# Optimization experiments

Measured on AMD Instinct MI355X. Metric: run time of the kernel, lower is better.

## Reference

```python
import jax, jax.numpy as jnp
import numpy as np

OUTDIM = 10
STRIDES = (2, 2, 1)
PADS = (2, 2, 1)  # int((k-1)/2) for k=5,5,3
LEAK = 0.2


def _conv(x, w, b, s, p):
    y = jax.lax.conv_general_dilated(x, w, (s, s), [(p, p), (p, p)],
                                     dimension_numbers=('NCHW', 'OIHW', 'NCHW'))
    return y + b[None, :, None, None]


def _grid(outdim):
    off = (jnp.arange(outdim, dtype=jnp.float32) - (outdim - 1) / 2.0) / outdim
    gx = jnp.broadcast_to(off[None, :], (outdim, outdim))  # varies along j (x)
    gy = jnp.broadcast_to(off[:, None], (outdim, outdim))  # varies along i (y)
    return jnp.stack([gx, gy], axis=-1)  # [od, od, 2]


def _bilinear(img, x, y):
    # img: [C,H,W]; x,y: [N] float. Faithful to original (x clamped by H, y by W).
    H, W = img.shape[-2], img.shape[-1]
    x0 = jnp.floor(x).astype(jnp.int32); x1 = x0 + 1
    y0 = jnp.floor(y).astype(jnp.int32); y1 = y0 + 1
    x0 = jnp.clip(x0, 0, H - 1); x1 = jnp.clip(x1, 0, H - 1)
    y0 = jnp.clip(y0, 0, W - 1); y1 = jnp.clip(y1, 0, W - 1)
    Ia = img[:, y0, x0]; Ib = img[:, y1, x0]; Ic = img[:, y0, x1]; Id = img[:, y1, x1]
    x0f = x0.astype(x.dtype); x1f = x1.astype(x.dtype)
    y0f = y0.astype(y.dtype); y1f = y1.astype(y.dtype)
    step = jnp.clip((x1f - x0f) * (y1f - y0f), 0.001, 2.0)
    inv = 1.0 / step
    wa = (x1f - x) * (y1f - y) * inv
    wb = (x1f - x) * (y - y0f) * inv
    wc = (x - x0f) * (y1f - y) * inv
    wd = (x - x0f) * (y - y0f) * inv
    return Ia * wa + Ib * wb + Ic * wc + Id * wd  # [C, N]


def _roi_one(feat, roi, gg):
    # feat: [C,H,W]; roi: [R,7]
    W1, W2 = roi[:, 2:3], roi[:, 3:4]
    H1, H2 = roi[:, 4:5], roi[:, 5:6]
    psi = roi[:, 6:7]
    WH = jnp.concatenate([W1 + W2, H1 + H2], axis=-1)          # [R,2]
    offset = jnp.concatenate([(W1 - W2) / 2, (H1 - H2) / 2], axis=-1)
    s, c = jnp.sin(psi), jnp.cos(psi)                          # [R,1]
    rotM = jnp.stack([jnp.concatenate([c, -s], -1),
                      jnp.concatenate([s, c], -1)], axis=-2)   # [R,2,2]
    ggi = gg[None] * WH[:, None, None, :] - offset[:, None, None, :]  # [R,od,od,2]
    ggi = jnp.einsum('rijk,rkl->rijl', ggi, rotM) + roi[:, None, None, 0:2]
    xs = ggi[..., 0].reshape(-1)
    ys = ggi[..., 1].reshape(-1)
    samp = _bilinear(feat, xs, ys)                             # [C, R*od*od]
    R, C = roi.shape[0], feat.shape[0]
    # faithful to original .view(R, C, od, od) applied to the [C, N] buffer
    return samp.reshape(R, C, OUTDIM, OUTDIM)


def setup_inputs() -> dict:
    key = jax.random.key(0)
    ks = jax.random.split(key, 12)
    B, R = 32, 32
    x = jax.random.normal(ks[0], (B, 3, 224, 224), dtype=jnp.float32)
    u = jax.random.uniform(ks[1], (B, R, 7), dtype=jnp.float32)
    lo = jnp.array([5., 5., 1., 1., 1., 1., -np.pi], dtype=jnp.float32)
    hi = jnp.array([51., 51., 8., 8., 8., 8., np.pi], dtype=jnp.float32)
    ROI = lo + u * (hi - lo)  # coords in 56x56 feature-map frame
    w1 = jax.random.normal(ks[2], (32, 3, 5, 5), dtype=jnp.float32) * 0.05
    b1 = jnp.zeros((32,), dtype=jnp.float32)
    w2 = jax.random.normal(ks[3], (64, 32, 5, 5), dtype=jnp.float32) * 0.05
    b2 = jnp.zeros((64,), dtype=jnp.float32)
    w3 = jax.random.normal(ks[4], (128, 64, 3, 3), dtype=jnp.float32) * 0.05
    b3 = jnp.zeros((128,), dtype=jnp.float32)
    fc_w = jax.random.normal(ks[5], (256, OUTDIM * OUTDIM * 128), dtype=jnp.float32) * 0.01
    fc_b = jnp.zeros((256,), dtype=jnp.float32)
    return {'x': x, 'ROI': ROI, 'w1': w1, 'b1': b1, 'w2': w2, 'b2': b2,
            'w3': w3, 'b3': b3, 'fc_w': fc_w, 'fc_b': fc_b}


def reference(x, ROI, w1, b1, w2, b2, w3, b3, fc_w, fc_b):
    for (w, b, s, p) in ((w1, b1, STRIDES[0], PADS[0]),
                         (w2, b2, STRIDES[1], PADS[1]),
                         (w3, b3, STRIDES[2], PADS[2])):
        x = jax.nn.leaky_relu(_conv(x, w, b, s, p), LEAK)
    gg = _grid(OUTDIM)
    roi_feat = jax.vmap(lambda f, r: _roi_one(f, r, gg))(x, ROI)  # [B,R,C,od,od]
    B, R = roi_feat.shape[0], roi_feat.shape[1]
    flat = roi_feat.reshape(B, R, -1)
    return flat @ fc_w.T + fc_b  # [B, R, 256]
```

## Files before the change

### kernel.cpp

```cpp
#include <hip/hip_runtime.h>
#include <hip/hip_bf16.h>

#define LEAK 0.2f

__device__ __forceinline__ float lrelu(float a) { return a > 0.0f ? a : LEAK * a; }

typedef __attribute__((ext_vector_type(8))) short short8;
typedef __attribute__((ext_vector_type(4))) float f32x4;

__device__ __forceinline__ unsigned short bf16_hi_bits(float x) {
    unsigned u = __builtin_bit_cast(unsigned, x);
    unsigned r = u + 0x7fffu + ((u >> 16) & 1u);
    return (unsigned short)(r >> 16);
}
__device__ __forceinline__ float bf16_to_f32(unsigned short h) {
    unsigned u = ((unsigned)h) << 16;
    return __builtin_bit_cast(float, u);
}
__device__ __forceinline__ unsigned pack_bf16pair(float x) {
    unsigned short h = bf16_hi_bits(x);
    float lo = x - bf16_to_f32(h);
    return (unsigned)h | ((unsigned)bf16_hi_bits(lo) << 16);
}

__device__ __forceinline__ unsigned pack_lo16(unsigned o, unsigned e) {
    return __builtin_amdgcn_perm(o, e, 0x05040100u);
}
__device__ __forceinline__ unsigned pack_hi16(unsigned o, unsigned e) {
    return __builtin_amdgcn_perm(o, e, 0x07060302u);
}

template<int CO, int KIN, int KP>
__global__ __launch_bounds__(256) void wtr_pack_k(const float* __restrict__ w,
                                                  unsigned* __restrict__ wTp) {
    int i = blockIdx.x * 256 + threadIdx.x;
    if (i >= KP * CO) return;
    int k = i / CO, co = i % CO;
    float x = (k < KIN) ? w[(size_t)co * KIN + k] : 0.0f;
    wTp[i] = pack_bf16pair(x);
}

__global__ __launch_bounds__(256) void split_pack_k(const float* __restrict__ src,
                                                    unsigned* __restrict__ dst, int n) {
    for (int i = blockIdx.x * 256 + threadIdx.x; i < n; i += gridDim.x * 256) {
        dst[i] = pack_bf16pair(src[i]);
    }
}

__global__ __launch_bounds__(256, 4) void conv1_mfma_k(
    const unsigned* __restrict__ src,
    const unsigned* __restrict__ wp,
    const float* __restrict__ bias,
    unsigned* __restrict__ outp)
{
    __shared__ unsigned ldsu[6400];
    __shared__ int offtab[96];
    short* const lds = (short*)ldsu;

    const int tid  = threadIdx.x;
    const int lane = tid & 63;
    const int wv   = tid >> 6;
    const int bx   = blockIdx.x;
    const int bz   = blockIdx.y;

    if (tid < 96) {
        int k = min(tid, 74);
        int ci = k / 25, r = k - ci * 25;
        int kh = r / 5, kw = r - kh * 5;
        offtab[tid] = (ci * 228 + kh) * 228 + kw;
    }
    __syncthreads();

    const int brow = tid & 127, half = tid >> 7;
    const int bn   = bx * 128 + brow;
    const int boh  = bn / 112, bow = bn % 112;
    const unsigned* __restrict__ bsrc =
        src + ((size_t)(bz * 3) * 228 + boh * 2) * 228 + bow * 2;
    const int arow = tid & 31, ks = (tid >> 5) & 3;

    unsigned Bu[16], Au[8];
    auto gather = [&](int it) {
        const int k0 = it * 32;
#pragma unroll
        for (int c = 0; c < 2; ++c) {
            int kb = k0 + (half * 2 + c) * 8;
            int4 o0 = *(const int4*)&offtab[kb];
            int4 o1 = *(const int4*)&offtab[kb + 4];
            Bu[c * 8 + 0] = bsrc[o0.x]; Bu[c * 8 + 1] = bsrc[o0.y];
            Bu[c * 8 + 2] = bsrc[o0.z]; Bu[c * 8 + 3] = bsrc[o0.w];
            Bu[c * 8 + 4] = bsrc[o1.x]; Bu[c * 8 + 5] = bsrc[o1.y];
            Bu[c * 8 + 6] = bsrc[o1.z]; Bu[c * 8 + 7] = bsrc[o1.w];
        }
        if (tid < 128) {
            const unsigned* __restrict__ wk = wp + (size_t)(k0 + ks * 8) * 32 + arow;
#pragma unroll
            for (int j = 0; j < 8; ++j) Au[j] = wk[j * 32];
        }
    };

    f32x4 acc[2][2] = {};
    const int r15 = lane & 15, kg = lane >> 4;

    gather(0);
    for (int it = 0; it < 3; ++it) {
        {
            uint4 vh, vl;
#pragma unroll
            for (int c = 0; c < 2; ++c) {
                vh.x = pack_lo16(Bu[c*8+1], Bu[c*8+0]); vl.x = pack_hi16(Bu[c*8+1], Bu[c*8+0]);
                vh.y = pack_lo16(Bu[c*8+3], Bu[c*8+2]); vl.y = pack_hi16(Bu[c*8+3], Bu[c*8+2]);
                vh.z = pack_lo16(Bu[c*8+5], Bu[c*8+4]); vl.z = pack_hi16(Bu[c*8+5], Bu[c*8+4]);
                vh.w = pack_lo16(Bu[c*8+7], Bu[c*8+6]); vl.w = pack_hi16(Bu[c*8+7], Bu[c*8+6]);
                *(uint4*)&ldsu[1280 + brow * 20 + (half * 2 + c) * 4] = vh;
                *(uint4*)&ldsu[3840 + brow * 20 + (half * 2 + c) * 4] = vl;
            }
            if (tid < 128) {
                vh.x = pack_lo16(Au[1], Au[0]); vl.x = pack_hi16(Au[1], Au[0]);
                vh.y = pack_lo16(Au[3], Au[2]); vl.y = pack_hi16(Au[3], Au[2]);
                vh.z = pack_lo16(Au[5], Au[4]); vl.z = pack_hi16(Au[5], Au[4]);
                vh.w = pack_lo16(Au[7], Au[6]); vl.w = pack_hi16(Au[7], Au[6]);
                *(uint4*)&ldsu[arow * 20 + ks * 4]       = vh;
                *(uint4*)&ldsu[640 + arow * 20 + ks * 4] = vl;
            }
        }
        __syncthreads();
        if (it + 1 < 3) gather(it + 1);

        const short* AsH = lds;
        const short* AsL = lds + 1280;
        const short* BsH = lds + 2560;
        const short* BsL = lds + 7680;
        short8 aH[2], aL[2], bH[2], bL[2];
#pragma unroll
        for (int tq = 0; tq < 2; ++tq) {
            const int ra = (tq * 16 + r15) * 40 + kg * 8;
            aH[tq] = *(const short8*)&AsH[ra];
            aL[tq] = *(const short8*)&AsL[ra];
            const int rb = (wv * 32 + tq * 16 + r15) * 40 + kg * 8;
            bH[tq] = *(const short8*)&BsH[rb];
            bL[tq] = *(const short8*)&BsL[rb];
        }
#pragma unroll
        for (int ct = 0; ct < 2; ++ct)
#pragma unroll
            for (int pt = 0; pt < 2; ++pt) {
                acc[ct][pt] = __builtin_amdgcn_mfma_f32_16x16x32_bf16(aH[ct], bH[pt], acc[ct][pt], 0, 0, 0);
                acc[ct][pt] = __builtin_amdgcn_mfma_f32_16x16x32_bf16(aH[ct], bL[pt], acc[ct][pt], 0, 0, 0);
                acc[ct][pt] = __builtin_amdgcn_mfma_f32_16x16x32_bf16(aL[ct], bH[pt], acc[ct][pt], 0, 0, 0);
            }
        __syncthreads();
    }

#pragma unroll
    for (int ct = 0; ct < 2; ++ct)
#pragma unroll
        for (int pt = 0; pt < 2; ++pt)
#pragma unroll
            for (int rg = 0; rg < 4; ++rg) {
                int co = ct * 16 + kg * 4 + rg;
                int px = bx * 128 + wv * 32 + pt * 16 + r15;
                int poh = px / 112, pw_ = px % 112;
                float v = acc[ct][pt][rg] + bias[co];
                outp[((size_t)(bz * 32 + co) * 116 + poh + 2) * 120 + pw_ + 4] =
                    pack_bf16pair(lrelu(v));
            }
}

template<int CI, int ST, int KH, int KW, int KP,
         int PIH, int PIW, int LP,
         int CO, int OW, int OSH, int OSW, int OR0, int OC0, bool POUT>
__global__ __launch_bounds__(256, 4) void conv_mfma_k(
    const unsigned* __restrict__ src,
    const unsigned* __restrict__ wp,
    const float* __restrict__ bias,
    void* __restrict__ outv)
{
    constexpr int KT = KP / 32;
    __shared__ unsigned ldsu[5120];
    __shared__ int offtab[KP];
    short* const lds = (short*)ldsu;

    const int tid  = threadIdx.x;
    const int lane = tid & 63;
    const int wv   = tid >> 6;
    const int bx   = blockIdx.x;
    const int by   = blockIdx.y;
    const int bz   = blockIdx.z;

    for (int k = tid; k < KP; k += 256) {
        int ci = k / (KH * KW), r = k - ci * (KH * KW);
        int kh = r / KW, kw = r - kh * KW;
        offtab[k] = (ci * PIH + kh) * PIW + kw;
    }
    __syncthreads();

    const int row = lane;
    const int n   = bx * 64 + row;
    const int oh  = n / OW, ow = n % OW;
    const unsigned* __restrict__ bsrc =
        src + ((size_t)(bz * CI) * PIH + oh * ST) * PIW + ow * ST + LP;
    const unsigned* __restrict__ wsrc = wp + (size_t)(wv * 8) * CO + by * 64 + row;

    unsigned Au[8], Bu[8];
    auto gather = [&](int it) {
        const int k0 = it * 32 + wv * 8;
        int4 o0 = *(const int4*)&offtab[k0];
        int4 o1 = *(const int4*)&offtab[k0 + 4];
        const unsigned* __restrict__ wk = wsrc + (size_t)it * 32 * CO;
#pragma unroll
        for (int j = 0; j < 8; ++j) Au[j] = wk[j * CO];
        Bu[0] = bsrc[o0.x]; Bu[1] = bsrc[o0.y]; Bu[2] = bsrc[o0.z]; Bu[3] = bsrc[o0.w];
        Bu[4] = bsrc[o1.x]; Bu[5] = bsrc[o1.y]; Bu[6] = bsrc[o1.z]; Bu[7] = bsrc[o1.w];
    };

    f32x4 acc[2][2] = {};

    const int cw = wv & 1, pw = wv >> 1;
    const int r15 = lane & 15, kg = lane >> 4;

    gather(0);
    for (int it = 0; it < KT; ++it) {
        {
            const int widx = row * 20 + wv * 4;
            uint4 vh, vl;
            vh.x = pack_lo16(Au[1], Au[0]); vl.x = pack_hi16(Au[1], Au[0]);
            vh.y = pack_lo16(Au[3], Au[2]); vl.y = pack_hi16(Au[3], Au[2]);
            vh.z = pack_lo16(Au[5], Au[4]); vl.z = pack_hi16(Au[5], Au[4]);
            vh.w = pack_lo16(Au[7], Au[6]); vl.w = pack_hi16(Au[7], Au[6]);
            *(uint4*)&ldsu[0 * 1280 + widx] = vh;
            *(uint4*)&ldsu[1 * 1280 + widx] = vl;
            vh.x = pack_lo16(Bu[1], Bu[0]); vl.x = pack_hi16(Bu[1], Bu[0]);
            vh.y = pack_lo16(Bu[3], Bu[2]); vl.y = pack_hi16(Bu[3], Bu[2]);
            vh.z = pack_lo16(Bu[5], Bu[4]); vl.z = pack_hi16(Bu[5], Bu[4]);
            vh.w = pack_lo16(Bu[7], Bu[6]); vl.w = pack_hi16(Bu[7], Bu[6]);
            *(uint4*)&ldsu[2 * 1280 + widx] = vh;
            *(uint4*)&ldsu[3 * 1280 + widx] = vl;
        }
        __syncthreads();
        if (it + 1 < KT) gather(it + 1);

        const short* AsH = lds + 0 * 2560;
        const short* AsL = lds + 1 * 2560;
        const short* BsH = lds + 2 * 2560;
        const short* BsL = lds + 3 * 2560;
        short8 aH[2], aL[2], bH[2], bL[2];
#pragma unroll
        for (int tq = 0; tq < 2; ++tq) {
            const int ra = (cw * 32 + tq * 16 + r15) * 40 + kg * 8;
            aH[tq] = *(const short8*)&AsH[ra];
            aL[tq] = *(const short8*)&AsL[ra];
            const int rb = (pw * 32 + tq * 16 + r15) * 40 + kg * 8;
            bH[tq] = *(const short8*)&BsH[rb];
            bL[tq] = *(const short8*)&BsL[rb];
        }
#pragma unroll
        for (int ct = 0; ct < 2; ++ct)
#pragma unroll
            for (int pt = 0; pt < 2; ++pt) {
                acc[ct][pt] = __builtin_amdgcn_mfma_f32_16x16x32_bf16(aH[ct], bH[pt], acc[ct][pt], 0, 0, 0);
                acc[ct][pt] = __builtin_amdgcn_mfma_f32_16x16x32_bf16(aH[ct], bL[pt], acc[ct][pt], 0, 0, 0);
                acc[ct][pt] = __builtin_amdgcn_mfma_f32_16x16x32_bf16(aL[ct], bH[pt], acc[ct][pt], 0, 0, 0);
            }
        __syncthreads();
    }

#pragma unroll
    for (int ct = 0; ct < 2; ++ct)
#pragma unroll
        for (int pt = 0; pt < 2; ++pt)
#pragma unroll
            for (int rg = 0; rg < 4; ++rg) {
                int co = by * 64 + cw * 32 + ct * 16 + kg * 4 + rg;
                int px = bx * 64 + pw * 32 + pt * 16 + r15;
                int poh = px / OW, pow_ = px % OW;
                float v = lrelu(acc[ct][pt][rg] + bias[co]);
                size_t off = ((size_t)(bz * CO + co) * OSH + (poh + OR0)) * OSW + (pow_ + OC0);
                if (POUT) ((unsigned*)outv)[off] = pack_bf16pair(v);
                else      ((float*)outv)[off]    = v;
            }
}

__global__ __launch_bounds__(256, 4) void fc_mfma_k(
    const unsigned* __restrict__ Sp,
    const unsigned* __restrict__ Wp,
    float* __restrict__ part)
{
    __shared__ unsigned ldsu[7680];
    short* const lds = (short*)ldsu;

    const int tid  = threadIdx.x;
    const int lane = tid & 63;
    const int wv   = tid >> 6;
    const int bn = blockIdx.x, bm = blockIdx.y, ks = blockIdx.z;

    const int ra = tid & 127, ca = tid >> 7;
    const int rb = tid & 63,  cb = tid >> 6;
    const unsigned* __restrict__ aptr = Sp + (size_t)(bm * 128 + ra) * 12800 + ks * 800;
    const unsigned* __restrict__ bptr = Wp + (size_t)(bn * 64 + rb) * 12800 + ks * 800;

    unsigned Au[16], Bu[8];
    auto gather = [&](int it) {
        const int k0 = it * 32;
#pragma unroll
        for (int j = 0; j < 8; ++j) {
            Au[j]     = aptr[k0 + ca * 8 + j];
            Au[8 + j] = aptr[k0 + (ca + 2) * 8 + j];
            Bu[j]     = bptr[k0 + cb * 8 + j];
        }
    };

    f32x4 acc[2][4] = {};
    const int r15 = lane & 15, kg = lane >> 4;

    gather(0);
    for (int it = 0; it < 25; ++it) {
        {
            uint4 vh, vl;
            vh.x = pack_lo16(Au[1], Au[0]); vl.x = pack_hi16(Au[1], Au[0]);
            vh.y = pack_lo16(Au[3], Au[2]); vl.y = pack_hi16(Au[3], Au[2]);
            vh.z = pack_lo16(Au[5], Au[4]); vl.z = pack_hi16(Au[5], Au[4]);
            vh.w = pack_lo16(Au[7], Au[6]); vl.w = pack_hi16(Au[7], Au[6]);
            *(uint4*)&ldsu[ra * 20 + ca * 4]        = vh;
            *(uint4*)&ldsu[2560 + ra * 20 + ca * 4] = vl;
            vh.x = pack_lo16(Au[9],  Au[8]);  vl.x = pack_hi16(Au[9],  Au[8]);
            vh.y = pack_lo16(Au[11], Au[10]); vl.y = pack_hi16(Au[11], Au[10]);
            vh.z = pack_lo16(Au[13], Au[12]); vl.z = pack_hi16(Au[13], Au[12]);
            vh.w = pack_lo16(Au[15], Au[14]); vl.w = pack_hi16(Au[15], Au[14]);
            *(uint4*)&ldsu[ra * 20 + (ca + 2) * 4]        = vh;
            *(uint4*)&ldsu[2560 + ra * 20 + (ca + 2) * 4] = vl;
            vh.x = pack_lo16(Bu[1], Bu[0]); vl.x = pack_hi16(Bu[1], Bu[0]);
            vh.y = pack_lo16(Bu[3], Bu[2]); vl.y = pack_hi16(Bu[3], Bu[2]);
            vh.z = pack_lo16(Bu[5], Bu[4]); vl.z = pack_hi16(Bu[5], Bu[4]);
            vh.w = pack_lo16(Bu[7], Bu[6]); vl.w = pack_hi16(Bu[7], Bu[6]);
            *(uint4*)&ldsu[5120 + rb * 20 + cb * 4] = vh;
            *(uint4*)&ldsu[6400 + rb * 20 + cb * 4] = vl;
        }
        __syncthreads();
        if (it + 1 < 25) gather(it + 1);

        const short* AsH = lds;
        const short* AsL = AsH + 5120;
        const short* BsH = AsH + 10240;
        const short* BsL = AsH + 12800;
        short8 aH[2], aL[2], bH[4], bL[4];
#pragma unroll
        for (int mq = 0; mq < 2; ++mq) {
            const int rr = (wv * 32 + mq * 16 + r15) * 40 + kg * 8;
            aH[mq] = *(const short8*)&AsH[rr];
            aL[mq] = *(const short8*)&AsL[rr];
        }
#pragma unroll
        for (int nq = 0; nq < 4; ++nq) {
            const int rr = (nq * 16 + r15) * 40 + kg * 8;
            bH[nq] = *(const short8*)&BsH[rr];
            bL[nq] = *(const short8*)&BsL[rr];
        }
#pragma unroll
        for (int mq = 0; mq < 2; ++mq)
#pragma unroll
            for (int nq = 0; nq < 4; ++nq) {
                acc[mq][nq] = __builtin_amdgcn_mfma_f32_16x16x32_bf16(aH[mq], bH[nq], acc[mq][nq], 0, 0, 0);
                acc[mq][nq] = __builtin_amdgcn_mfma_f32_16x16x32_bf16(aH[mq], bL[nq], acc[mq][nq], 0, 0, 0);
                acc[mq][nq] = __builtin_amdgcn_mfma_f32_16x16x32_bf16(aL[mq], bH[nq], acc[mq][nq], 0, 0, 0);
            }
        __syncthreads();
    }

    float* __restrict__ po = part + (size_t)ks * 262144;
#pragma unroll
    for (int mq = 0; mq < 2; ++mq)
#pragma unroll
        for (int nq = 0; nq < 4; ++nq)
#pragma unroll
            for (int rg = 0; rg < 4; ++rg) {
                int m = bm * 128 + wv * 32 + mq * 16 + kg * 4 + rg;
                int ncol = bn * 64 + nq * 16 + r15;
                po[(size_t)m * 256 + ncol] = acc[mq][nq][rg];
            }
}

__global__ __launch_bounds__(256) void pad_x_k(const float* __restrict__ x,
                                               unsigned* __restrict__ xp) {
    int blk = blockIdx.x;
    int r4 = blk % 57, ic = blk / 57;
    int wid = threadIdx.x >> 6, lane = threadIdx.x & 63;
    int row = r4 * 4 + wid;
    const float* __restrict__ src = x + (size_t)ic * 224 * 224 + (size_t)(row - 2) * 224;
    unsigned* __restrict__ dst = xp + (size_t)ic * 228 * 228 + (size_t)row * 228;
    bool rok = (row >= 2) && (row < 226);
    for (int c = lane; c < 228; c += 64) {
        float v = 0.0f;
        if (rok && c >= 2 && c < 226) v = src[c - 2];
        dst[c] = pack_bf16pair(v);
    }
}

__global__ __launch_bounds__(256) void zb_c1p_k(float* __restrict__ p) {
    float* base = p + (size_t)blockIdx.x * (116 * 120);
    for (int t = threadIdx.x; t < 928; t += 256) {
        int idx;
        if (t < 480) {
            int r = t / 120, c = t - r * 120;
            int row = (r < 2) ? r : r + 112;
            idx = row * 120 + c;
        } else {
            int s = t - 480;
            int r = s >> 2, c = s & 3;
            int col = (c < 2) ? (c + 2) : (c + 114);
            idx = (r + 2) * 120 + col;
        }
        base[idx] = 0.0f;
    }
}

__global__ __launch_bounds__(64) void zb_c2p_k(float* __restrict__ p) {
    float* base = p + (size_t)blockIdx.x * (58 * 64);
    for (int t = threadIdx.x; t < 240; t += 64) {
        int idx;
        if (t < 128) {
            int r = t >> 6, c = t & 63;
            idx = (r ? 57 : 0) * 64 + c;
        } else {
            int s = t - 128;
            int r = (s >> 1) + 1;
            idx = r * 64 + ((s & 1) ? 60 : 3);
        }
        base[idx] = 0.0f;
    }
}

__global__ __launch_bounds__(256) void roi_k(const float* __restrict__ feat,
                                             const float* __restrict__ roi,
                                             unsigned* __restrict__ S) {
    int b = blockIdx.x >> 5;
    int r = blockIdx.x & 31;
    const float* rr = roi + (size_t)(b * 32 + r) * 7;

    __shared__ int   offA[100], offB[100], offC[100], offD[100];
    __shared__ float wA[100], wB[100], wC[100], wD[100];

    int tid = threadIdx.x;
    if (tid < 100) {
        int i = tid / 10, j = tid % 10;
        float cx = rr[0], cy = rr[1];
        float W1 = rr[2], W2 = rr[3], H1 = rr[4], H2 = rr[5], psi = rr[6];
        float offx = ((float)j - 4.5f) / 10.0f;
        float offy = ((float)i - 4.5f) / 10.0f;
        float gx = offx * (W1 + W2) - (W1 - W2) * 0.5f;
        float gy = offy * (H1 + H2) - (H1 - H2) * 0.5f;
        float sn = sinf(psi), cs = cosf(psi);
        float xs = gx * cs + gy * sn + cx;
        float ys = -gx * sn + gy * cs + cy;

        float x0f = floorf(xs), y0f = floorf(ys);
        int x0 = (int)x0f, x1 = x0 + 1;
        int y0 = (int)y0f, y1 = y0 + 1;
        x0 = min(max(x0, 0), 55); x1 = min(max(x1, 0), 55);
        y0 = min(max(y0, 0), 55); y1 = min(max(y1, 0), 55);
        float fx0 = (float)x0, fx1 = (float)x1;
        float fy0 = (float)y0, fy1 = (float)y1;
        float step = (fx1 - fx0) * (fy1 - fy0);
        step = fminf(fmaxf(step, 0.001f), 2.0f);
        float inv = 1.0f / step;
        wA[tid] = (fx1 - xs) * (fy1 - ys) * inv;
        wB[tid] = (fx1 - xs) * (ys - fy0) * inv;
        wC[tid] = (xs - fx0) * (fy1 - ys) * inv;
        wD[tid] = (xs - fx0) * (ys - fy0) * inv;
        offA[tid] = y0 * 56 + x0;
        offB[tid] = y1 * 56 + x0;
        offC[tid] = y0 * 56 + x1;
        offD[tid] = y1 * 56 + x1;
    }
    __syncthreads();

    const float* __restrict__ fb = feat + (size_t)b * 128 * 3136;
    unsigned* __restrict__ outb = S + ((size_t)b * 128 * 32 + r) * 100;
    int c = tid / 100;
    int p = tid - c * 100;
    for (int t = tid; t < 12800; t += 256) {
        const float* f = fb + c * 3136;
        float v = wA[p] * f[offA[p]] + wB[p] * f[offB[p]] +
                  wC[p] * f[offC[p]] + wD[p] * f[offD[p]];
        outb[(size_t)c * 3200 + p] = pack_bf16pair(v);
        p += 56; c += 2;
        if (p >= 100) { p -= 100; ++c; }
    }
}

__global__ __launch_bounds__(256) void fc2_reduce_k(const float* __restrict__ part,
                                                    const float* __restrict__ bias,
                                                    float* __restrict__ out) {
    int i = blockIdx.x * 256 + threadIdx.x;
    float s = bias[i & 255];
    for (int ks = 0; ks < 16; ++ks) s += part[(size_t)ks * 262144 + i];
    out[i] = s;
}

extern "C" void kernel_launch(void* const* d_in, const int* in_sizes, int n_in,
                              void* d_out, int out_size, void* d_ws, size_t ws_size,
                              hipStream_t stream) {
    const float* x   = (const float*)d_in[0];
    const float* ROI = (const float*)d_in[1];
    const float* w1  = (const float*)d_in[2];
    const float* b1  = (const float*)d_in[3];
    const float* w2  = (const float*)d_in[4];
    const float* b2  = (const float*)d_in[5];
    const float* w3  = (const float*)d_in[6];
    const float* b3  = (const float*)d_in[7];
    const float* fcw = (const float*)d_in[8];
    const float* fcb = (const float*)d_in[9];
    float* out = (float*)d_out;

    char* ws = (char*)d_ws;
    unsigned* c1p  = (unsigned*)(ws);
    unsigned* c2p  = (unsigned*)(ws + 57016320);
    unsigned* xpad = (unsigned*)(ws + 87425024);
    unsigned* wT1p = (unsigned*)(ws + 107386880);
    unsigned* wT2p = (unsigned*)(ws + 107399168);
    unsigned* wT3p = (unsigned*)(ws + 107603968);
    float* c3   = (float*)(ws);
    unsigned* S = (unsigned*)(ws + 57016320);
    unsigned* wfcp = (unsigned*)(ws);
    float* part = (float*)(ws + 16777216);

    wtr_pack_k<32, 75, 96><<<12, 256, 0, stream>>>(w1, wT1p);
    wtr_pack_k<64, 800, 800><<<200, 256, 0, stream>>>(w2, wT2p);
    wtr_pack_k<128, 576, 576><<<288, 256, 0, stream>>>(w3, wT3p);
    pad_x_k<<<32 * 3 * 57, 256, 0, stream>>>(x, xpad);
    zb_c1p_k<<<1024, 256, 0, stream>>>((float*)c1p);
    zb_c2p_k<<<2048, 64, 0, stream>>>((float*)c2p);

    conv1_mfma_k<<<dim3(98, 32), 256, 0, stream>>>(xpad, wT1p, b1, c1p);

    conv_mfma_k<32, 2, 5, 5, 800, 116, 120, 2, 64, 56, 58, 64, 1, 4, true>
        <<<dim3(49, 1, 32), 256, 0, stream>>>(c1p, wT2p, b2, c2p);

    conv_mfma_k<64, 1, 3, 3, 576, 58, 64, 3, 128, 56, 56, 56, 0, 0, false>
        <<<dim3(49, 2, 32), 256, 0, stream>>>(c2p, wT3p, b3, c3);

    roi_k<<<1024, 256, 0, stream>>>(c3, ROI, S);
    split_pack_k<<<4096, 256, 0, stream>>>(fcw, wfcp, 3276800);
    fc_mfma_k<<<dim3(4, 8, 16), 256, 0, stream>>>(S, wfcp, part);
    fc2_reduce_k<<<1024, 256, 0, stream>>>(part, fcb, out);
}
```

Before: 371.2 us.

## Widen conv MFMA pixel tile to 128 and flatten batch into pixel dimension

The generic conv2/conv3 implicit-GEMM kernel now covers 128 output pixels per block instead of 64, with each wave computing a 32x64 tile. The batch grid dimension is folded into a flat pixel index (PPI = 3136 pixels per image), so the image index is derived per pixel. This doubles reuse of each weight tile loaded into LDS and halves the block count. The cost is more LDS (7680 words), more accumulators and gather registers per thread, which may lower occupancy.

After: 382.1 us. 1.03x slower.

```diff
diff --git a/kernel.cpp b/kernel.cpp
--- a/kernel.cpp
+++ b/kernel.cpp
@@ -168,7 +168,7 @@
 
 template<int CI, int ST, int KH, int KW, int KP,
          int PIH, int PIW, int LP,
-         int CO, int OW, int OSH, int OSW, int OR0, int OC0, bool POUT>
+         int CO, int OW, int PPI, int OSH, int OSW, int OR0, int OC0, bool POUT>
 __global__ __launch_bounds__(256, 4) void conv_mfma_k(
     const unsigned* __restrict__ src,
     const unsigned* __restrict__ wp,
@@ -176,7 +176,7 @@
     void* __restrict__ outv)
 {
     constexpr int KT = KP / 32;
-    __shared__ unsigned ldsu[5120];
+    __shared__ unsigned ldsu[7680];
     __shared__ int offtab[KP];
     short* const lds = (short*)ldsu;
 
@@ -185,7 +185,6 @@
     const int wv   = tid >> 6;
     const int bx   = blockIdx.x;
     const int by   = blockIdx.y;
-    const int bz   = blockIdx.z;
 
     for (int k = tid; k < KP; k += 256) {
         int ci = k / (KH * KW), r = k - ci * (KH * KW);
@@ -194,26 +193,30 @@
     }
     __syncthreads();
 
-    const int row = lane;
-    const int n   = bx * 64 + row;
-    const int oh  = n / OW, ow = n % OW;
+    const int brow = tid & 127, khalf = tid >> 7;
+    const int bn   = bx * 128 + brow;
+    const int bimg = bn / PPI, brem = bn % PPI;
+    const int boh  = brem / OW, bow = brem % OW;
     const unsigned* __restrict__ bsrc =
-        src + ((size_t)(bz * CI) * PIH + oh * ST) * PIW + ow * ST + LP;
-    const unsigned* __restrict__ wsrc = wp + (size_t)(wv * 8) * CO + by * 64 + row;
-
-    unsigned Au[8], Bu[8];
+        src + ((size_t)(bimg * CI) * PIH + boh * ST) * PIW + bow * ST + LP;
+    const int arow = tid & 63, aks = tid >> 6;
+    const unsigned* __restrict__ wsrc = wp + (size_t)(aks * 8) * CO + by * 64 + arow;
+
+    unsigned Bu[16], Au[8];
     auto gather = [&](int it) {
-        const int k0 = it * 32 + wv * 8;
-        int4 o0 = *(const int4*)&offtab[k0];
-        int4 o1 = *(const int4*)&offtab[k0 + 4];
+        const int k0 = it * 32;
+#pragma unroll
+        for (int c = 0; c < 4; ++c) {
+            int4 o = *(const int4*)&offtab[k0 + khalf * 16 + c * 4];
+            Bu[c * 4 + 0] = bsrc[o.x]; Bu[c * 4 + 1] = bsrc[o.y];
+            Bu[c * 4 + 2] = bsrc[o.z]; Bu[c * 4 + 3] = bsrc[o.w];
+        }
         const unsigned* __restrict__ wk = wsrc + (size_t)it * 32 * CO;
 #pragma unroll
         for (int j = 0; j < 8; ++j) Au[j] = wk[j * CO];
-        Bu[0] = bsrc[o0.x]; Bu[1] = bsrc[o0.y]; Bu[2] = bsrc[o0.z]; Bu[3] = bsrc[o0.w];
-        Bu[4] = bsrc[o1.x]; Bu[5] = bsrc[o1.y]; Bu[6] = bsrc[o1.z]; Bu[7] = bsrc[o1.w];
     };
 
-    f32x4 acc[2][2] = {};
+    f32x4 acc[2][4] = {};
 
     const int cw = wv & 1, pw = wv >> 1;
     const int r15 = lane & 15, kg = lane >> 4;
@@ -221,42 +224,47 @@
     gather(0);
     for (int it = 0; it < KT; ++it) {
         {
-            const int widx = row * 20 + wv * 4;
             uint4 vh, vl;
             vh.x = pack_lo16(Au[1], Au[0]); vl.x = pack_hi16(Au[1], Au[0]);
             vh.y = pack_lo16(Au[3], Au[2]); vl.y = pack_hi16(Au[3], Au[2]);
             vh.z = pack_lo16(Au[5], Au[4]); vl.z = pack_hi16(Au[5], Au[4]);
             vh.w = pack_lo16(Au[7], Au[6]); vl.w = pack_hi16(Au[7], Au[6]);
-            *(uint4*)&ldsu[0 * 1280 + widx] = vh;
-            *(uint4*)&ldsu[1 * 1280 + widx] = vl;
-            vh.x = pack_lo16(Bu[1], Bu[0]); vl.x = pack_hi16(Bu[1], Bu[0]);
-            vh.y = pack_lo16(Bu[3], Bu[2]); vl.y = pack_hi16(Bu[3], Bu[2]);
-            vh.z = pack_lo16(Bu[5], Bu[4]); vl.z = pack_hi16(Bu[5], Bu[4]);
-            vh.w = pack_lo16(Bu[7], Bu[6]); vl.w = pack_hi16(Bu[7], Bu[6]);
-            *(uint4*)&ldsu[2 * 1280 + widx] = vh;
-            *(uint4*)&ldsu[3 * 1280 + widx] = vl;
+            *(uint4*)&ldsu[arow * 20 + aks * 4]        = vh;
+            *(uint4*)&ldsu[1280 + arow * 20 + aks * 4] = vl;
+#pragma unroll
+            for (int c = 0; c < 2; ++c) {
+                vh.x = pack_lo16(Bu[c*8+1], Bu[c*8+0]); vl.x = pack_hi16(Bu[c*8+1], Bu[c*8+0]);
+                vh.y = pack_lo16(Bu[c*8+3], Bu[c*8+2]); vl.y = pack_hi16(Bu[c*8+3], Bu[c*8+2]);
+                vh.z = pack_lo16(Bu[c*8+5], Bu[c*8+4]); vl.z = pack_hi16(Bu[c*8+5], Bu[c*8+4]);
+                vh.w = pack_lo16(Bu[c*8+7], Bu[c*8+6]); vl.w = pack_hi16(Bu[c*8+7], Bu[c*8+6]);
+                *(uint4*)&ldsu[2560 + brow * 20 + khalf * 8 + c * 4] = vh;
+                *(uint4*)&ldsu[5120 + brow * 20 + khalf * 8 + c * 4] = vl;
+            }
         }
         __syncthreads();
         if (it + 1 < KT) gather(it + 1);
 
-        const short* AsH = lds + 0 * 2560;
-        const short* AsL = lds + 1 * 2560;
-        const short* BsH = lds + 2 * 2560;
-        const short* BsL = lds + 3 * 2560;
-        short8 aH[2], aL[2], bH[2], bL[2];
+        const short* AsH = lds;
+        const short* AsL = lds + 2560;
+        const short* BsH = lds + 5120;
+        const short* BsL = lds + 10240;
+        short8 aH[2], aL[2], bH[4], bL[4];
 #pragma unroll
         for (int tq = 0; tq < 2; ++tq) {
             const int ra = (cw * 32 + tq * 16 + r15) * 40 + kg * 8;
             aH[tq] = *(const short8*)&AsH[ra];
             aL[tq] = *(const short8*)&AsL[ra];
-            const int rb = (pw * 32 + tq * 16 + r15) * 40 + kg * 8;
-            bH[tq] = *(const short8*)&BsH[rb];
-            bL[tq] = *(const short8*)&BsL[rb];
+        }
+#pragma unroll
+        for (int nq = 0; nq < 4; ++nq) {
+            const int rb = (pw * 64 + nq * 16 + r15) * 40 + kg * 8;
+            bH[nq] = *(const short8*)&BsH[rb];
+            bL[nq] = *(const short8*)&BsL[rb];
         }
 #pragma unroll
         for (int ct = 0; ct < 2; ++ct)
 #pragma unroll
-            for (int pt = 0; pt < 2; ++pt) {
+            for (int pt = 0; pt < 4; ++pt) {
                 acc[ct][pt] = __builtin_amdgcn_mfma_f32_16x16x32_bf16(aH[ct], bH[pt], acc[ct][pt], 0, 0, 0);
                 acc[ct][pt] = __builtin_amdgcn_mfma_f32_16x16x32_bf16(aH[ct], bL[pt], acc[ct][pt], 0, 0, 0);
                 acc[ct][pt] = __builtin_amdgcn_mfma_f32_16x16x32_bf16(aL[ct], bH[pt], acc[ct][pt], 0, 0, 0);
@@ -267,14 +275,15 @@
 #pragma unroll
     for (int ct = 0; ct < 2; ++ct)
 #pragma unroll
-        for (int pt = 0; pt < 2; ++pt)
+        for (int pt = 0; pt < 4; ++pt)
 #pragma unroll
             for (int rg = 0; rg < 4; ++rg) {
-                int co = by * 64 + cw * 32 + ct * 16 + kg * 4 + rg;
-                int px = bx * 64 + pw * 32 + pt * 16 + r15;
-                int poh = px / OW, pow_ = px % OW;
+                int co  = by * 64 + cw * 32 + ct * 16 + kg * 4 + rg;
+                int pxg = bx * 128 + pw * 64 + pt * 16 + r15;
+                int img = pxg / PPI, rem = pxg % PPI;
+                int poh = rem / OW, pow_ = rem % OW;
                 float v = lrelu(acc[ct][pt][rg] + bias[co]);
-                size_t off = ((size_t)(bz * CO + co) * OSH + (poh + OR0)) * OSW + (pow_ + OC0);
+                size_t off = ((size_t)(img * CO + co) * OSH + (poh + OR0)) * OSW + (pow_ + OC0);
                 if (POUT) ((unsigned*)outv)[off] = pack_bf16pair(v);
                 else      ((float*)outv)[off]    = v;
             }
@@ -532,11 +541,11 @@
 
     conv1_mfma_k<<<dim3(98, 32), 256, 0, stream>>>(xpad, wT1p, b1, c1p);
 
-    conv_mfma_k<32, 2, 5, 5, 800, 116, 120, 2, 64, 56, 58, 64, 1, 4, true>
-        <<<dim3(49, 1, 32), 256, 0, stream>>>(c1p, wT2p, b2, c2p);
-
-    conv_mfma_k<64, 1, 3, 3, 576, 58, 64, 3, 128, 56, 56, 56, 0, 0, false>
-        <<<dim3(49, 2, 32), 256, 0, stream>>>(c2p, wT3p, b3, c3);
+    conv_mfma_k<32, 2, 5, 5, 800, 116, 120, 2, 64, 56, 3136, 58, 64, 1, 4, true>
+        <<<dim3(784, 1), 256, 0, stream>>>(c1p, wT2p, b2, c2p);
+
+    conv_mfma_k<64, 1, 3, 3, 576, 58, 64, 3, 128, 56, 3136, 56, 56, 0, 0, false>
+        <<<dim3(784, 2), 256, 0, stream>>>(c2p, wT3p, b3, c3);
 
     roi_k<<<1024, 256, 0, stream>>>(c3, ROI, S);
     split_pack_k<<<4096, 256, 0, stream>>>(fcw, wfcp, 3276800);
```
